# Kernel optimization log

Measured on AMD Instinct MI355X. Metric: run time of the kernel, lower is better.

The kernel has to match this reference:

```python
import jax, jax.numpy as jnp
import numpy as np

N_NODES = 50000
N_EDGES = 800000
N_GRAPHS = 256
D_FEAT = 96
HIDDEN = 32


def setup_inputs() -> dict:
    key = jax.random.key(0)
    ks = jax.random.split(key, 8)
    x = jax.random.normal(ks[0], (N_NODES, D_FEAT), dtype=jnp.float32)
    edge_index = jax.random.randint(ks[1], (2, N_EDGES), 0, N_NODES, dtype=jnp.int64)
    batch = jnp.sort(jax.random.randint(ks[2], (N_NODES,), 0, N_GRAPHS, dtype=jnp.int64))
    W1 = jax.random.normal(ks[3], (D_FEAT, HIDDEN), dtype=jnp.float32) * 0.05
    b1 = jnp.zeros((HIDDEN,), dtype=jnp.float32)
    W2 = jax.random.normal(ks[4], (HIDDEN, HIDDEN), dtype=jnp.float32) * 0.05
    b2 = jnp.zeros((HIDDEN,), dtype=jnp.float32)
    Wc = jax.random.normal(ks[5], (HIDDEN, 2), dtype=jnp.float32) * 0.05
    bc = jnp.zeros((2,), dtype=jnp.float32)
    return {"x": x, "edge_index": edge_index, "batch": batch,
            "W1": W1, "b1": b1, "W2": W2, "b2": b2, "Wc": Wc, "bc": bc}


def reference(x, edge_index, batch, W1, b1, W2, b2, Wc, bc):
    src, dst = edge_index[0], edge_index[1]
    # GIN aggregation (eps=0): h_i = x_i + sum_{j -> i} x_j, scatter-add over edges
    agg = jax.ops.segment_sum(x[src], dst, num_segments=N_NODES)
    h = agg + x
    # 2-layer MLP inside GINConv
    h = jnp.maximum(h @ W1 + b1, 0.0) @ W2 + b2
    # outer ReLU (F.relu in forward)
    h = jnp.maximum(h, 0.0)
    # global mean pool per graph
    sums = jax.ops.segment_sum(h, batch, num_segments=N_GRAPHS)          # [G, H]
    counts = jax.ops.segment_sum(jnp.ones((N_NODES,), h.dtype), batch,
                                 num_segments=N_GRAPHS)                   # [G]
    pooled = sums / jnp.maximum(counts, 1.0)[:, None]
    return pooled @ Wc + bc  # [G, 2]
```

## Files before the change

kernel.cpp:

```cpp
#include <hip/hip_runtime.h>
#include <hip/hip_fp16.h>

#define N_NODES 50000
#define N_EDGES 800000
#define N_GRAPHS 256
#define D_FEAT 96
#define HIDDEN 32

#define NB 196
#define PB 400
#define PCHUNK 2000
#define SEGCAP 64
#define GWIN 16
#define LCAP 6400
#define XT 64
#define XBLK 782
#define XS_STRIDE 97
#define DUMMY_NODE N_NODES

__global__ void __launch_bounds__(256)
k_front(const float* __restrict__ x, const float* __restrict__ W1,
        __half* __restrict__ y16,
        const int* __restrict__ src, const int* __restrict__ dst,
        unsigned int* __restrict__ binned, unsigned short* __restrict__ cnt,
        float* __restrict__ sums, float* __restrict__ counts) {
    int blk = blockIdx.x;
    int tid = threadIdx.x;
    if (blk < PB) {
        __shared__ int hcur[NB];
        for (int i = tid; i < NB; i += 256) hcur[i] = 0;
        __syncthreads();

        int e0 = blk * PCHUNK, e1 = e0 + PCHUNK;
        for (int e = e0 + tid; e < e1; e += 256) {
            int sn = src[e];
            int d  = dst[e];
            int b  = d >> 8;
            int pos = atomicAdd(&hcur[b], 1);
            if (pos < SEGCAP)
                binned[((size_t)b * PB + blk) * SEGCAP + pos] =
                    (unsigned)sn | ((unsigned)(d & 255) << 16);
        }
        __syncthreads();

        for (int i = tid; i < NB; i += 256) {
            int c = hcur[i]; if (c > SEGCAP) c = SEGCAP;
            cnt[i * PB + blk] = (unsigned short)c;
        }
    } else {
        __shared__ float xs[XT * XS_STRIDE];
        int xb = blk - PB;
        int n0 = xb * XT;
        int nn = N_NODES - n0; if (nn > XT) nn = XT;

        int gid = xb * 256 + tid;
        if (gid < N_GRAPHS * HIDDEN) sums[gid] = 0.f;
        if (gid < N_GRAPHS) counts[gid] = 0.f;
        if (xb == 0 && tid < HIDDEN)
            y16[(size_t)DUMMY_NODE * HIDDEN + tid] = __float2half(0.f);

        const float4* xsrc = (const float4*)(x + (size_t)n0 * D_FEAT);
        int nf4 = nn * (D_FEAT / 4);
        for (int idx = tid; idx < nf4; idx += 256) {
            int ln = (idx * 2731) >> 16;
            int k4 = idx - ln * 24;
            float4 v = xsrc[idx];
            float* dp = &xs[ln * XS_STRIDE + k4 * 4];
            dp[0] = v.x; dp[1] = v.y; dp[2] = v.z; dp[3] = v.w;
        }
        __syncthreads();

        int lane = tid & 63;
        int f0 = (tid >> 6) << 3;
        f0 = __builtin_amdgcn_readfirstlane(f0);

        if (lane < nn) {
            const float* xr = &xs[lane * XS_STRIDE];
            const float4* W1v = (const float4*)W1;
            float acc[8];
#pragma unroll
            for (int j = 0; j < 8; ++j) acc[j] = 0.f;
#pragma unroll
            for (int k = 0; k < D_FEAT; ++k) {
                float xv = xr[k];
                float4 wa = W1v[k * 8 + (f0 >> 2)];
                float4 wb = W1v[k * 8 + (f0 >> 2) + 1];
                acc[0] = fmaf(xv, wa.x, acc[0]);
                acc[1] = fmaf(xv, wa.y, acc[1]);
                acc[2] = fmaf(xv, wa.z, acc[2]);
                acc[3] = fmaf(xv, wa.w, acc[3]);
                acc[4] = fmaf(xv, wb.x, acc[4]);
                acc[5] = fmaf(xv, wb.y, acc[5]);
                acc[6] = fmaf(xv, wb.z, acc[6]);
                acc[7] = fmaf(xv, wb.w, acc[7]);
            }
            __half2 h01 = __floats2half2_rn(acc[0], acc[1]);
            __half2 h23 = __floats2half2_rn(acc[2], acc[3]);
            __half2 h45 = __floats2half2_rn(acc[4], acc[5]);
            __half2 h67 = __floats2half2_rn(acc[6], acc[7]);
            float4 pack;
            pack.x = __uint_as_float(*(const unsigned*)&h01);
            pack.y = __uint_as_float(*(const unsigned*)&h23);
            pack.z = __uint_as_float(*(const unsigned*)&h45);
            pack.w = __uint_as_float(*(const unsigned*)&h67);
            *(float4*)&y16[(size_t)(n0 + lane) * HIDDEN + f0] = pack;
        }
    }
}

__global__ void __launch_bounds__(1024)
k_agg(const unsigned int* __restrict__ binned, const unsigned short* __restrict__ cnt,
      const __half* __restrict__ y16, const int* __restrict__ batch,
      const float* __restrict__ b1, const float* __restrict__ W2,
      const float* __restrict__ b2,
      float* __restrict__ sums, float* __restrict__ counts) {
    __shared__ unsigned int list[LCAP];
    __shared__ unsigned short list2[LCAP];
    __shared__ unsigned int sA[512], sB[512];
    __shared__ unsigned short cs[PB];
    __shared__ unsigned int sOfs[PB];
    __shared__ unsigned int ncnt[256];
    __shared__ unsigned int offs[257];
    __shared__ unsigned int cur[256];
    __shared__ float w2s[HIDDEN * HIDDEN];
    __shared__ float accs[GWIN * HIDDEN];
    __shared__ float cntsl[GWIN];

    int tid = threadIdx.x;
    int bin = blockIdx.x;
    if (tid < 256) ncnt[tid] = 0;
    for (int i = tid; i < HIDDEN * HIDDEN; i += 1024) w2s[i] = W2[i];
    if (tid < GWIN * HIDDEN) accs[tid] = 0.f;
    if (tid < GWIN) cntsl[tid] = 0.f;
    if (tid < 512) {
        unsigned c = (tid < PB) ? (unsigned)cnt[bin * PB + tid] : 0u;
        if (tid < PB) cs[tid] = (unsigned short)c;
        sA[tid] = c;
    }
    __syncthreads();

    unsigned *ps = sA, *pd = sB;
    for (int d = 1; d < 512; d <<= 1) {
        if (tid < 512) { unsigned v = ps[tid]; if (tid >= d) v += ps[tid - d]; pd[tid] = v; }
        __syncthreads();
        unsigned* t = ps; ps = pd; pd = t;
    }
    if (tid < PB) sOfs[tid] = tid ? ps[tid - 1] : 0u;
    int ecount = (int)ps[PB - 1];
    if (ecount > LCAP) ecount = LCAP;
    __syncthreads();

    const unsigned int* ebase = binned + (size_t)bin * PB * SEGCAP;
    for (int idx = tid; idx < PB * SEGCAP; idx += 1024) {
        int s = idx >> 6;
        int i = idx & 63;
        if (i < (int)cs[s]) {
            unsigned pos = sOfs[s] + i;
            if (pos < LCAP) list[pos] = ebase[idx];
        }
    }
    __syncthreads();

    for (int e = tid; e < ecount; e += 1024)
        atomicAdd(&ncnt[list[e] >> 16], 1u);
    __syncthreads();

    if (tid < 256) sA[tid] = (ncnt[tid] + 7u) & ~7u;
    __syncthreads();
    ps = sA; pd = sB;
    for (int d = 1; d < 256; d <<= 1) {
        if (tid < 256) { unsigned v = ps[tid]; if (tid >= d) v += ps[tid - d]; pd[tid] = v; }
        __syncthreads();
        unsigned* t = ps; ps = pd; pd = t;
    }
    if (tid < 256) {
        offs[tid + 1] = ps[tid];
        cur[tid] = tid ? ps[tid - 1] : 0u;
    }
    if (tid == 0) offs[0] = 0;
    __syncthreads();

    for (int e = tid; e < ecount; e += 1024) {
        unsigned p = list[e];
        unsigned pos = atomicAdd(&cur[p >> 16], 1u);
        if (pos < LCAP) list2[pos] = (unsigned short)(p & 0xFFFFu);
    }
    __syncthreads();
    if (tid < 256) {
        unsigned i0 = cur[tid], i1 = offs[tid + 1];
        for (unsigned i = i0; i < i1 && i < LCAP; ++i)
            list2[i] = (unsigned short)DUMMY_NODE;
    }
    __syncthreads();

    int node0 = bin << 8;
    int nn = N_NODES - node0; if (nn > 256) nn = 256;
    int g = tid >> 5;
    int f = tid & 31;
    int gfirst = batch[node0];

    for (int ln = g * 8; ln < g * 8 + 8; ++ln) {
        if (ln >= nn) break;
        int node = node0 + ln;
        float acc = __half2float(y16[(size_t)node * HIDDEN + f]);
        int j = offs[ln], jend = offs[ln + 1];
        for (; j < jend; j += 8) {
            ushort4 qa = *(const ushort4*)&list2[j];
            ushort4 qb = *(const ushort4*)&list2[j + 4];
            float a0 = __half2float(y16[(size_t)qa.x * HIDDEN + f]);
            float a1 = __half2float(y16[(size_t)qa.y * HIDDEN + f]);
            float a2 = __half2float(y16[(size_t)qa.z * HIDDEN + f]);
            float a3 = __half2float(y16[(size_t)qa.w * HIDDEN + f]);
            float a4 = __half2float(y16[(size_t)qb.x * HIDDEN + f]);
            float a5 = __half2float(y16[(size_t)qb.y * HIDDEN + f]);
            float a6 = __half2float(y16[(size_t)qb.z * HIDDEN + f]);
            float a7 = __half2float(y16[(size_t)qb.w * HIDDEN + f]);
            acc += ((a0 + a1) + (a2 + a3)) + ((a4 + a5) + (a6 + a7));
        }

        float h1 = fmaxf(acc + b1[f], 0.f);
        float h2 = b2[f];
#pragma unroll
        for (int k = 0; k < HIDDEN; ++k)
            h2 = fmaf(__shfl(h1, k, 32), w2s[k * HIDDEN + f], h2);
        float h = fmaxf(h2, 0.f);

        int gr = batch[node];
        int b = gr - gfirst;
        if (b < GWIN) {
            atomicAdd(&accs[b * HIDDEN + f], h);
            if (f == 0) atomicAdd(&cntsl[b], 1.f);
        } else {
            atomicAdd(&sums[(size_t)gr * HIDDEN + f], h);
            if (f == 0) atomicAdd(&counts[gr], 1.f);
        }
    }
    __syncthreads();

    for (int i = tid; i < GWIN * HIDDEN; i += 1024) {
        float v = accs[i];
        if (v != 0.f) atomicAdd(&sums[(size_t)gfirst * HIDDEN + i], v);
    }
    if (tid < GWIN) {
        float c = cntsl[tid];
        if (c != 0.f) atomicAdd(&counts[gfirst + tid], c);
    }
}

__global__ void k_out(const float* __restrict__ sums, const float* __restrict__ counts,
                      const float* __restrict__ Wc, const float* __restrict__ bc,
                      float* __restrict__ out) {
    int g = threadIdx.x;
    if (g >= N_GRAPHS) return;
    float inv = 1.f / fmaxf(counts[g], 1.f);
    float o0 = bc[0], o1 = bc[1];
#pragma unroll
    for (int k = 0; k < HIDDEN; ++k) {
        float p = sums[(size_t)g * HIDDEN + k] * inv;
        o0 = fmaf(p, Wc[k * 2 + 0], o0);
        o1 = fmaf(p, Wc[k * 2 + 1], o1);
    }
    out[g * 2 + 0] = o0;
    out[g * 2 + 1] = o1;
}

extern "C" void kernel_launch(void* const* d_in, const int* in_sizes, int n_in,
                              void* d_out, int out_size, void* d_ws, size_t ws_size,
                              hipStream_t stream) {
    const float* x     = (const float*)d_in[0];
    const int*   ei    = (const int*)d_in[1];
    const int*   batch = (const int*)d_in[2];
    const float* W1    = (const float*)d_in[3];
    const float* b1    = (const float*)d_in[4];
    const float* W2    = (const float*)d_in[5];
    const float* b2    = (const float*)d_in[6];
    const float* Wc    = (const float*)d_in[7];
    const float* bc    = (const float*)d_in[8];
    float* out = (float*)d_out;

    char* ws = (char*)d_ws;
    float*          sums   = (float*)ws;
    float*          counts = (float*)(ws + 32768);
    unsigned short* cnt    = (unsigned short*)(ws + 33792);
    unsigned int*   binned = (unsigned int*)(ws + 190592);
    __half*         y16    = (__half*)(ws + 20260992);

    k_front<<<PB + XBLK, 256, 0, stream>>>(
        x, W1, y16, ei, ei + N_EDGES, binned, cnt, sums, counts);

    k_agg<<<NB, 1024, 0, stream>>>(binned, cnt, y16, batch,
                                   b1, W2, b2, sums, counts);

    k_out<<<1, 256, 0, stream>>>(sums, counts, Wc, bc, out);
}
```

Before: 133.6 us.

## Replace padded per-bin edge segments with compact locally sorted runs and smaller bins

The partition stage now counting-sorts each edge chunk by destination bin in shared memory and writes a dense sorted chunk, plus a packed offset/count per (bin, chunk). Before, it wrote fixed 64-slot padded segments. The aggregation kernel gathers contiguous runs using those offsets instead of scanning a sparse padded array. Bins shrink from 256 to 128 nodes, so nearly twice as many aggregation blocks run. This is meant to cut wasted memory traffic from padded segments and improve occupancy, at the cost of extra scans and serial per-thread run copies.

```diff
diff --git a/kernel.cpp b/kernel.cpp
--- a/kernel.cpp
+++ b/kernel.cpp
@@ -7,12 +7,13 @@
 #define D_FEAT 96
 #define HIDDEN 32
 
-#define NB 196
-#define PB 400
-#define PCHUNK 2000
-#define SEGCAP 64
-#define GWIN 16
-#define LCAP 6400
+#define NB 391
+#define PB 625
+#define PCHUNK 1280
+#define EPT 5
+#define GWIN 8
+#define LCAP 2560
+#define L2CAP 3584
 #define XT 64
 #define XBLK 782
 #define XS_STRIDE 97
@@ -22,31 +23,61 @@
 k_front(const float* __restrict__ x, const float* __restrict__ W1,
         __half* __restrict__ y16,
         const int* __restrict__ src, const int* __restrict__ dst,
-        unsigned int* __restrict__ binned, unsigned short* __restrict__ cnt,
+        unsigned int* __restrict__ binned, unsigned int* __restrict__ co,
         float* __restrict__ sums, float* __restrict__ counts) {
     int blk = blockIdx.x;
     int tid = threadIdx.x;
     if (blk < PB) {
-        __shared__ int hcur[NB];
-        for (int i = tid; i < NB; i += 256) hcur[i] = 0;
-        __syncthreads();
-
-        int e0 = blk * PCHUNK, e1 = e0 + PCHUNK;
-        for (int e = e0 + tid; e < e1; e += 256) {
-            int sn = src[e];
-            int d  = dst[e];
-            int b  = d >> 8;
-            int pos = atomicAdd(&hcur[b], 1);
-            if (pos < SEGCAP)
-                binned[((size_t)b * PB + blk) * SEGCAP + pos] =
-                    (unsigned)sn | ((unsigned)(d & 255) << 16);
-        }
-        __syncthreads();
-
+        __shared__ unsigned int sorted[PCHUNK];
+        __shared__ unsigned int sA[512];
+        __shared__ unsigned int sB[512];
+        __shared__ unsigned int lcur[NB];
+
+        for (int i = tid; i < 512; i += 256) sA[i] = 0;
+        __syncthreads();
+
+        int e0 = blk * PCHUNK;
+        unsigned int pay[EPT];
+        int bb[EPT];
+#pragma unroll
+        for (int i = 0; i < EPT; ++i) {
+            int e = e0 + i * 256 + tid;
+            int s = src[e];
+            int d = dst[e];
+            int b = d >> 7;
+            pay[i] = (unsigned)s | ((unsigned)(d & 127) << 16);
+            bb[i] = b;
+            atomicAdd(&sA[b], 1u);
+        }
+        __syncthreads();
+
+        unsigned *ps = sA, *pd = sB;
+        for (int d = 1; d < 512; d <<= 1) {
+            for (int idx = tid; idx < 512; idx += 256) {
+                unsigned v = ps[idx];
+                if (idx >= d) v += ps[idx - d];
+                pd[idx] = v;
+            }
+            __syncthreads();
+            unsigned* t = ps; ps = pd; pd = t;
+        }
         for (int i = tid; i < NB; i += 256) {
-            int c = hcur[i]; if (c > SEGCAP) c = SEGCAP;
-            cnt[i * PB + blk] = (unsigned short)c;
-        }
+            unsigned incl = ps[i];
+            unsigned excl = i ? ps[i - 1] : 0u;
+            lcur[i] = excl;
+            co[(size_t)i * PB + blk] = excl | ((incl - excl) << 16);
+        }
+        __syncthreads();
+
+#pragma unroll
+        for (int i = 0; i < EPT; ++i) {
+            unsigned pos = atomicAdd(&lcur[bb[i]], 1u);
+            sorted[pos] = pay[i];
+        }
+        __syncthreads();
+
+        for (int i = tid; i < PCHUNK; i += 256)
+            binned[(size_t)blk * PCHUNK + i] = sorted[i];
     } else {
         __shared__ float xs[XT * XS_STRIDE];
         int xb = blk - PB;
@@ -109,54 +140,55 @@
 }
 
 __global__ void __launch_bounds__(1024)
-k_agg(const unsigned int* __restrict__ binned, const unsigned short* __restrict__ cnt,
+k_agg(const unsigned int* __restrict__ binned, const unsigned int* __restrict__ co,
       const __half* __restrict__ y16, const int* __restrict__ batch,
       const float* __restrict__ b1, const float* __restrict__ W2,
       const float* __restrict__ b2,
       float* __restrict__ sums, float* __restrict__ counts) {
     __shared__ unsigned int list[LCAP];
-    __shared__ unsigned short list2[LCAP];
-    __shared__ unsigned int sA[512], sB[512];
-    __shared__ unsigned short cs[PB];
-    __shared__ unsigned int sOfs[PB];
-    __shared__ unsigned int ncnt[256];
-    __shared__ unsigned int offs[257];
-    __shared__ unsigned int cur[256];
+    __shared__ unsigned short list2[L2CAP];
+    __shared__ unsigned int sA[1024], sB[1024];
+    __shared__ unsigned int ncnt[128];
+    __shared__ unsigned int offs[129];
+    __shared__ unsigned int cur[128];
     __shared__ float w2s[HIDDEN * HIDDEN];
     __shared__ float accs[GWIN * HIDDEN];
     __shared__ float cntsl[GWIN];
 
     int tid = threadIdx.x;
     int bin = blockIdx.x;
-    if (tid < 256) ncnt[tid] = 0;
+    if (tid < 128) ncnt[tid] = 0;
     for (int i = tid; i < HIDDEN * HIDDEN; i += 1024) w2s[i] = W2[i];
     if (tid < GWIN * HIDDEN) accs[tid] = 0.f;
     if (tid < GWIN) cntsl[tid] = 0.f;
-    if (tid < 512) {
-        unsigned c = (tid < PB) ? (unsigned)cnt[bin * PB + tid] : 0u;
-        if (tid < PB) cs[tid] = (unsigned short)c;
-        sA[tid] = c;
-    }
+
+    unsigned myofs = 0, mycnt = 0;
+    if (tid < PB) {
+        unsigned w = co[(size_t)bin * PB + tid];
+        myofs = w & 0xFFFFu;
+        mycnt = w >> 16;
+    }
+    sA[tid] = mycnt;
     __syncthreads();
 
     unsigned *ps = sA, *pd = sB;
-    for (int d = 1; d < 512; d <<= 1) {
-        if (tid < 512) { unsigned v = ps[tid]; if (tid >= d) v += ps[tid - d]; pd[tid] = v; }
+    for (int d = 1; d < 1024; d <<= 1) {
+        unsigned v = ps[tid];
+        if (tid >= d) v += ps[tid - d];
+        pd[tid] = v;
         __syncthreads();
         unsigned* t = ps; ps = pd; pd = t;
     }
-    if (tid < PB) sOfs[tid] = tid ? ps[tid - 1] : 0u;
     int ecount = (int)ps[PB - 1];
     if (ecount > LCAP) ecount = LCAP;
-    __syncthreads();
-
-    const unsigned int* ebase = binned + (size_t)bin * PB * SEGCAP;
-    for (int idx = tid; idx < PB * SEGCAP; idx += 1024) {
-        int s = idx >> 6;
-        int i = idx & 63;
-        if (i < (int)cs[s]) {
-            unsigned pos = sOfs[s] + i;
-            if (pos < LCAP) list[pos] = ebase[idx];
+    unsigned mybase = (tid < PB && tid > 0) ? ps[tid - 1] : 0u;
+    __syncthreads();
+
+    if (tid < PB) {
+        const unsigned int* run = binned + (size_t)tid * PCHUNK + myofs;
+        for (unsigned i = 0; i < mycnt; ++i) {
+            unsigned pos = mybase + i;
+            if (pos < LCAP) list[pos] = run[i];
         }
     }
     __syncthreads();
@@ -165,15 +197,15 @@
         atomicAdd(&ncnt[list[e] >> 16], 1u);
     __syncthreads();
 
-    if (tid < 256) sA[tid] = (ncnt[tid] + 7u) & ~7u;
+    if (tid < 128) sA[tid] = (ncnt[tid] + 7u) & ~7u;
     __syncthreads();
     ps = sA; pd = sB;
-    for (int d = 1; d < 256; d <<= 1) {
-        if (tid < 256) { unsigned v = ps[tid]; if (tid >= d) v += ps[tid - d]; pd[tid] = v; }
+    for (int d = 1; d < 128; d <<= 1) {
+        if (tid < 128) { unsigned v = ps[tid]; if (tid >= d) v += ps[tid - d]; pd[tid] = v; }
         __syncthreads();
         unsigned* t = ps; ps = pd; pd = t;
     }
-    if (tid < 256) {
+    if (tid < 128) {
         offs[tid + 1] = ps[tid];
         cur[tid] = tid ? ps[tid - 1] : 0u;
     }
@@ -183,23 +215,23 @@
     for (int e = tid; e < ecount; e += 1024) {
         unsigned p = list[e];
         unsigned pos = atomicAdd(&cur[p >> 16], 1u);
-        if (pos < LCAP) list2[pos] = (unsigned short)(p & 0xFFFFu);
-    }
-    __syncthreads();
-    if (tid < 256) {
+        if (pos < L2CAP) list2[pos] = (unsigned short)(p & 0xFFFFu);
+    }
+    __syncthreads();
+    if (tid < 128) {
         unsigned i0 = cur[tid], i1 = offs[tid + 1];
-        for (unsigned i = i0; i < i1 && i < LCAP; ++i)
+        for (unsigned i = i0; i < i1 && i < L2CAP; ++i)
             list2[i] = (unsigned short)DUMMY_NODE;
     }
     __syncthreads();
 
-    int node0 = bin << 8;
-    int nn = N_NODES - node0; if (nn > 256) nn = 256;
+    int node0 = bin << 7;
+    int nn = N_NODES - node0; if (nn > 128) nn = 128;
     int g = tid >> 5;
     int f = tid & 31;
     int gfirst = batch[node0];
 
-    for (int ln = g * 8; ln < g * 8 + 8; ++ln) {
+    for (int ln = g * 4; ln < g * 4 + 4; ++ln) {
         if (ln >= nn) break;
         int node = node0 + ln;
         float acc = __half2float(y16[(size_t)node * HIDDEN + f]);
@@ -279,16 +311,16 @@
     float* out = (float*)d_out;
 
     char* ws = (char*)d_ws;
-    float*          sums   = (float*)ws;
-    float*          counts = (float*)(ws + 32768);
-    unsigned short* cnt    = (unsigned short*)(ws + 33792);
-    unsigned int*   binned = (unsigned int*)(ws + 190592);
-    __half*         y16    = (__half*)(ws + 20260992);
+    float*        sums   = (float*)ws;
+    float*        counts = (float*)(ws + 32768);
+    unsigned int* co     = (unsigned int*)(ws + 33792);
+    unsigned int* binned = (unsigned int*)(ws + 1011456);
+    __half*       y16    = (__half*)(ws + 4211456);
 
     k_front<<<PB + XBLK, 256, 0, stream>>>(
-        x, W1, y16, ei, ei + N_EDGES, binned, cnt, sums, counts);
-
-    k_agg<<<NB, 1024, 0, stream>>>(binned, cnt, y16, batch,
+        x, W1, y16, ei, ei + N_EDGES, binned, co, sums, counts);
+
+    k_agg<<<NB, 1024, 0, stream>>>(binned, co, y16, batch,
                                    b1, W2, b2, sums, counts);
 
     k_out<<<1, 256, 0, stream>>>(sums, counts, Wc, bc, out);
```

Measured after the change: 136.1 us. No clear change (+1.9%).

## Bin edges by global cursor into compact per-bin lists, aggregate with LDS atomics

Applied to the files above, without the earlier changes.

The edge partitioning now does a local histogram, scan and sort per chunk, then reserves contiguous space per destination bin through global atomic cursors. This replaces the sparse fixed-capacity segment layout and the per-block scan/compaction work in the aggregation kernel. Aggregation now distributes edges evenly across warps and scatter-adds into an LDS accumulator with float atomics instead of a per-node CSR walk, which removes the second counting sort but adds shared-memory atomic contention. The change also adds a memset launch and uses nontemporal loads for x. Edges in a bin beyond LCAP are dropped.

```diff
diff --git a/kernel.cpp b/kernel.cpp
--- a/kernel.cpp
+++ b/kernel.cpp
@@ -7,48 +7,79 @@
 #define D_FEAT 96
 #define HIDDEN 32
 
-#define NB 196
-#define PB 400
-#define PCHUNK 2000
-#define SEGCAP 64
-#define GWIN 16
-#define LCAP 6400
+#define NBIN 250
+#define BINN 200
+#define PB 160
+#define PCHUNK 5000
+#define LCAP 4608
+#define GWIN 8
 #define XT 64
 #define XBLK 782
 #define XS_STRIDE 97
-#define DUMMY_NODE N_NODES
+
+typedef float vfloat4 __attribute__((ext_vector_type(4)));
+#define NTL(p) __builtin_nontemporal_load(p)
 
 __global__ void __launch_bounds__(256)
 k_front(const float* __restrict__ x, const float* __restrict__ W1,
         __half* __restrict__ y16,
         const int* __restrict__ src, const int* __restrict__ dst,
-        unsigned int* __restrict__ binned, unsigned short* __restrict__ cnt,
+        int* __restrict__ cursor, unsigned int* __restrict__ binned,
         float* __restrict__ sums, float* __restrict__ counts) {
+    __shared__ __align__(16) char smem[25088];
     int blk = blockIdx.x;
     int tid = threadIdx.x;
     if (blk < PB) {
-        __shared__ int hcur[NB];
-        for (int i = tid; i < NB; i += 256) hcur[i] = 0;
-        __syncthreads();
-
-        int e0 = blk * PCHUNK, e1 = e0 + PCHUNK;
-        for (int e = e0 + tid; e < e1; e += 256) {
-            int sn = src[e];
-            int d  = dst[e];
-            int b  = d >> 8;
-            int pos = atomicAdd(&hcur[b], 1);
-            if (pos < SEGCAP)
-                binned[((size_t)b * PB + blk) * SEGCAP + pos] =
-                    (unsigned)sn | ((unsigned)(d & 255) << 16);
-        }
-        __syncthreads();
-
-        for (int i = tid; i < NB; i += 256) {
-            int c = hcur[i]; if (c > SEGCAP) c = SEGCAP;
-            cnt[i * PB + blk] = (unsigned short)c;
+        unsigned int* sorted = (unsigned int*)smem;
+        unsigned int* hist   = (unsigned int*)(smem + 20000);
+        unsigned int* scanA  = (unsigned int*)(smem + 21000);
+        unsigned int* curb   = (unsigned int*)(smem + 22000);
+        unsigned int* gbase  = (unsigned int*)(smem + 23000);
+
+        for (int i = tid; i < NBIN; i += 256) hist[i] = 0;
+        __syncthreads();
+
+        int e0 = blk * PCHUNK;
+        for (int e = e0 + tid; e < e0 + PCHUNK; e += 256)
+            atomicAdd(&hist[dst[e] / BINN], 1u);
+        __syncthreads();
+
+        if (tid < NBIN) scanA[tid] = hist[tid];
+        __syncthreads();
+        for (int d = 1; d < NBIN; d <<= 1) {
+            unsigned v = 0;
+            if (tid < NBIN && tid >= d) v = scanA[tid - d];
+            __syncthreads();
+            if (tid < NBIN) scanA[tid] += v;
+            __syncthreads();
+        }
+
+        if (tid < NBIN) {
+            unsigned h = hist[tid];
+            gbase[tid] = h ? (unsigned)atomicAdd(&cursor[tid], (int)h) : 0u;
+            curb[tid] = scanA[tid] - h;
+        }
+        __syncthreads();
+
+        for (int e = e0 + tid; e < e0 + PCHUNK; e += 256) {
+            int s = src[e];
+            int d = dst[e];
+            int b = d / BINN;
+            unsigned pos = atomicAdd(&curb[b], 1u);
+            sorted[pos] = (unsigned)s | ((unsigned)d << 16);
+        }
+        __syncthreads();
+
+        for (int p = tid; p < PCHUNK; p += 256) {
+            unsigned w = sorted[p];
+            int b = (int)(w >> 16) / BINN;
+            unsigned excl = scanA[b] - hist[b];
+            unsigned pos = gbase[b] + ((unsigned)p - excl);
+            if (pos < LCAP)
+                binned[(size_t)b * LCAP + pos] = w;
         }
     } else {
-        __shared__ float xs[XT * XS_STRIDE];
+        float* xs = (float*)smem;
         int xb = blk - PB;
         int n0 = xb * XT;
         int nn = N_NODES - n0; if (nn > XT) nn = XT;
@@ -56,15 +87,13 @@
         int gid = xb * 256 + tid;
         if (gid < N_GRAPHS * HIDDEN) sums[gid] = 0.f;
         if (gid < N_GRAPHS) counts[gid] = 0.f;
-        if (xb == 0 && tid < HIDDEN)
-            y16[(size_t)DUMMY_NODE * HIDDEN + tid] = __float2half(0.f);
-
-        const float4* xsrc = (const float4*)(x + (size_t)n0 * D_FEAT);
+
+        const vfloat4* xsrc = (const vfloat4*)(x + (size_t)n0 * D_FEAT);
         int nf4 = nn * (D_FEAT / 4);
         for (int idx = tid; idx < nf4; idx += 256) {
             int ln = (idx * 2731) >> 16;
             int k4 = idx - ln * 24;
-            float4 v = xsrc[idx];
+            vfloat4 v = NTL(&xsrc[idx]);
             float* dp = &xs[ln * XS_STRIDE + k4 * 4];
             dp[0] = v.x; dp[1] = v.y; dp[2] = v.z; dp[3] = v.w;
         }
@@ -109,116 +138,75 @@
 }
 
 __global__ void __launch_bounds__(1024)
-k_agg(const unsigned int* __restrict__ binned, const unsigned short* __restrict__ cnt,
+k_agg(const unsigned int* __restrict__ binned, const int* __restrict__ cursor,
       const __half* __restrict__ y16, const int* __restrict__ batch,
       const float* __restrict__ b1, const float* __restrict__ W2,
       const float* __restrict__ b2,
       float* __restrict__ sums, float* __restrict__ counts) {
+    __shared__ float agg[BINN * HIDDEN];
     __shared__ unsigned int list[LCAP];
-    __shared__ unsigned short list2[LCAP];
-    __shared__ unsigned int sA[512], sB[512];
-    __shared__ unsigned short cs[PB];
-    __shared__ unsigned int sOfs[PB];
-    __shared__ unsigned int ncnt[256];
-    __shared__ unsigned int offs[257];
-    __shared__ unsigned int cur[256];
     __shared__ float w2s[HIDDEN * HIDDEN];
     __shared__ float accs[GWIN * HIDDEN];
     __shared__ float cntsl[GWIN];
 
     int tid = threadIdx.x;
     int bin = blockIdx.x;
-    if (tid < 256) ncnt[tid] = 0;
+    int node0 = bin * BINN;
+
+    for (int i = tid; i < BINN * HIDDEN; i += 1024) agg[i] = 0.f;
     for (int i = tid; i < HIDDEN * HIDDEN; i += 1024) w2s[i] = W2[i];
     if (tid < GWIN * HIDDEN) accs[tid] = 0.f;
     if (tid < GWIN) cntsl[tid] = 0.f;
-    if (tid < 512) {
-        unsigned c = (tid < PB) ? (unsigned)cnt[bin * PB + tid] : 0u;
-        if (tid < PB) cs[tid] = (unsigned short)c;
-        sA[tid] = c;
-    }
+
+    int ecount = cursor[bin];
+    if (ecount > LCAP) ecount = LCAP;
+    const unsigned int* eb = binned + (size_t)bin * LCAP;
+    for (int i = tid; i < ecount; i += 1024) list[i] = eb[i];
     __syncthreads();
 
-    unsigned *ps = sA, *pd = sB;
-    for (int d = 1; d < 512; d <<= 1) {
-        if (tid < 512) { unsigned v = ps[tid]; if (tid >= d) v += ps[tid - d]; pd[tid] = v; }
-        __syncthreads();
-        unsigned* t = ps; ps = pd; pd = t;
-    }
-    if (tid < PB) sOfs[tid] = tid ? ps[tid - 1] : 0u;
-    int ecount = (int)ps[PB - 1];
-    if (ecount > LCAP) ecount = LCAP;
-    __syncthreads();
-
-    const unsigned int* ebase = binned + (size_t)bin * PB * SEGCAP;
-    for (int idx = tid; idx < PB * SEGCAP; idx += 1024) {
-        int s = idx >> 6;
-        int i = idx & 63;
-        if (i < (int)cs[s]) {
-            unsigned pos = sOfs[s] + i;
-            if (pos < LCAP) list[pos] = ebase[idx];
-        }
-    }
-    __syncthreads();
-
-    for (int e = tid; e < ecount; e += 1024)
-        atomicAdd(&ncnt[list[e] >> 16], 1u);
-    __syncthreads();
-
-    if (tid < 256) sA[tid] = (ncnt[tid] + 7u) & ~7u;
-    __syncthreads();
-    ps = sA; pd = sB;
-    for (int d = 1; d < 256; d <<= 1) {
-        if (tid < 256) { unsigned v = ps[tid]; if (tid >= d) v += ps[tid - d]; pd[tid] = v; }
-        __syncthreads();
-        unsigned* t = ps; ps = pd; pd = t;
-    }
-    if (tid < 256) {
-        offs[tid + 1] = ps[tid];
-        cur[tid] = tid ? ps[tid - 1] : 0u;
-    }
-    if (tid == 0) offs[0] = 0;
-    __syncthreads();
-
-    for (int e = tid; e < ecount; e += 1024) {
-        unsigned p = list[e];
-        unsigned pos = atomicAdd(&cur[p >> 16], 1u);
-        if (pos < LCAP) list2[pos] = (unsigned short)(p & 0xFFFFu);
-    }
-    __syncthreads();
-    if (tid < 256) {
-        unsigned i0 = cur[tid], i1 = offs[tid + 1];
-        for (unsigned i = i0; i < i1 && i < LCAP; ++i)
-            list2[i] = (unsigned short)DUMMY_NODE;
-    }
-    __syncthreads();
-
-    int node0 = bin << 8;
-    int nn = N_NODES - node0; if (nn > 256) nn = 256;
     int g = tid >> 5;
     int f = tid & 31;
+
+    int chunk = (ecount + 31) >> 5;
+    int e0 = g * chunk;
+    int e1 = e0 + chunk; if (e1 > ecount) e1 = ecount;
+    for (int e = e0; e < e1; e += 8) {
+        int rem = e1 - e;
+        unsigned w0 = list[e];
+        unsigned w1 = (rem > 1) ? list[e + 1] : w0;
+        unsigned w2 = (rem > 2) ? list[e + 2] : w0;
+        unsigned w3 = (rem > 3) ? list[e + 3] : w0;
+        unsigned w4 = (rem > 4) ? list[e + 4] : w0;
+        unsigned w5 = (rem > 5) ? list[e + 5] : w0;
+        unsigned w6 = (rem > 6) ? list[e + 6] : w0;
+        unsigned w7 = (rem > 7) ? list[e + 7] : w0;
+        float a0 = __half2float(y16[(size_t)(w0 & 0xFFFFu) * HIDDEN + f]);
+        float a1 = __half2float(y16[(size_t)(w1 & 0xFFFFu) * HIDDEN + f]);
+        float a2 = __half2float(y16[(size_t)(w2 & 0xFFFFu) * HIDDEN + f]);
+        float a3 = __half2float(y16[(size_t)(w3 & 0xFFFFu) * HIDDEN + f]);
+        float a4 = __half2float(y16[(size_t)(w4 & 0xFFFFu) * HIDDEN + f]);
+        float a5 = __half2float(y16[(size_t)(w5 & 0xFFFFu) * HIDDEN + f]);
+        float a6 = __half2float(y16[(size_t)(w6 & 0xFFFFu) * HIDDEN + f]);
+        float a7 = __half2float(y16[(size_t)(w7 & 0xFFFFu) * HIDDEN + f]);
+        atomicAdd(&agg[((w0 >> 16) - node0) * HIDDEN + f], a0);
+        if (rem > 1) atomicAdd(&agg[((w1 >> 16) - node0) * HIDDEN + f], a1);
+        if (rem > 2) atomicAdd(&agg[((w2 >> 16) - node0) * HIDDEN + f], a2);
+        if (rem > 3) atomicAdd(&agg[((w3 >> 16) - node0) * HIDDEN + f], a3);
+        if (rem > 4) atomicAdd(&agg[((w4 >> 16) - node0) * HIDDEN + f], a4);
+        if (rem > 5) atomicAdd(&agg[((w5 >> 16) - node0) * HIDDEN + f], a5);
+        if (rem > 6) atomicAdd(&agg[((w6 >> 16) - node0) * HIDDEN + f], a6);
+        if (rem > 7) atomicAdd(&agg[((w7 >> 16) - node0) * HIDDEN + f], a7);
+    }
+    __syncthreads();
+
+    int nn = N_NODES - node0; if (nn > BINN) nn = BINN;
     int gfirst = batch[node0];
 
-    for (int ln = g * 8; ln < g * 8 + 8; ++ln) {
-        if (ln >= nn) break;
+    for (int ln = g; ln < nn; ln += 32) {
         int node = node0 + ln;
-        float acc = __half2float(y16[(size_t)node * HIDDEN + f]);
-        int j = offs[ln], jend = offs[ln + 1];
-        for (; j < jend; j += 8) {
-            ushort4 qa = *(const ushort4*)&list2[j];
-            ushort4 qb = *(const ushort4*)&list2[j + 4];
-            float a0 = __half2float(y16[(size_t)qa.x * HIDDEN + f]);
-            float a1 = __half2float(y16[(size_t)qa.y * HIDDEN + f]);
-            float a2 = __half2float(y16[(size_t)qa.z * HIDDEN + f]);
-            float a3 = __half2float(y16[(size_t)qa.w * HIDDEN + f]);
-            float a4 = __half2float(y16[(size_t)qb.x * HIDDEN + f]);
-            float a5 = __half2float(y16[(size_t)qb.y * HIDDEN + f]);
-            float a6 = __half2float(y16[(size_t)qb.z * HIDDEN + f]);
-            float a7 = __half2float(y16[(size_t)qb.w * HIDDEN + f]);
-            acc += ((a0 + a1) + (a2 + a3)) + ((a4 + a5) + (a6 + a7));
-        }
-
-        float h1 = fmaxf(acc + b1[f], 0.f);
+        float h1 = agg[ln * HIDDEN + f]
+                 + __half2float(y16[(size_t)node * HIDDEN + f]) + b1[f];
+        h1 = fmaxf(h1, 0.f);
         float h2 = b2[f];
 #pragma unroll
         for (int k = 0; k < HIDDEN; ++k)
@@ -279,17 +267,19 @@
     float* out = (float*)d_out;
 
     char* ws = (char*)d_ws;
-    float*          sums   = (float*)ws;
-    float*          counts = (float*)(ws + 32768);
-    unsigned short* cnt    = (unsigned short*)(ws + 33792);
-    unsigned int*   binned = (unsigned int*)(ws + 190592);
-    __half*         y16    = (__half*)(ws + 20260992);
+    int*          cursor = (int*)ws;
+    float*        sums   = (float*)(ws + 1024);
+    float*        counts = (float*)(ws + 33792);
+    unsigned int* binned = (unsigned int*)(ws + 34816);
+    __half*       y16    = (__half*)(ws + 4642816);
+
+    hipMemsetAsync(cursor, 0, 1024, stream);
 
     k_front<<<PB + XBLK, 256, 0, stream>>>(
-        x, W1, y16, ei, ei + N_EDGES, binned, cnt, sums, counts);
-
-    k_agg<<<NB, 1024, 0, stream>>>(binned, cnt, y16, batch,
-                                   b1, W2, b2, sums, counts);
+        x, W1, y16, ei, ei + N_EDGES, cursor, binned, sums, counts);
+
+    k_agg<<<NBIN, 1024, 0, stream>>>(binned, cursor, y16, batch,
+                                     b1, W2, b2, sums, counts);
 
     k_out<<<1, 256, 0, stream>>>(sums, counts, Wc, bc, out);
 }
```

Result: slower. 259.6 us (+94.3%).
